# Kernel optimization log

Hardware: AMD Instinct MI355X
Metric: run time of the kernel (lower is better)

Reference implementation:

```python
import jax, jax.numpy as jnp
import numpy as np

D = 768       # feature dim (LayerNorm([768]))
NCHAR = 96    # codebook rows (char_dic = zeros(96, 768))
EPS = 1e-5    # torch LayerNorm default eps
EMA = 0.1     # EMA update coefficient


def layer_norm(x, w, b):
    mu = jnp.mean(x, axis=-1, keepdims=True)
    var = jnp.mean((x - mu) ** 2, axis=-1, keepdims=True)
    return (x - mu) * jax.lax.rsqrt(var + EPS) * w + b


def setup_inputs() -> dict:
    key = jax.random.key(0)
    k1, k2, k3 = jax.random.split(key, 3)
    B, S = 128, 1024
    return {
        "input_f": jax.random.normal(k1, (B, S, D), dtype=jnp.float32),
        "char_dic": jax.random.normal(k2, (NCHAR, D), dtype=jnp.float32),
        "ln_w": jnp.ones((D,), dtype=jnp.float32),
        "ln_b": jnp.zeros((D,), dtype=jnp.float32),
        "target": jax.random.randint(k3, (B, S), 0, NCHAR),
    }


def reference(input_f, char_dic, ln_w, ln_b, target):
    x = layer_norm(input_f, ln_w, ln_b)              # [B, S, D]
    flat = x.reshape(-1, D)                          # [N, D]
    labels = target.reshape(-1)                      # [N]
    # per-label scatter-add of token embeddings
    tok_sums = jax.ops.segment_sum(flat, labels, num_segments=NCHAR)          # [96, D]
    counts = jax.ops.segment_sum(jnp.ones_like(labels, dtype=jnp.float32),
                                 labels, num_segments=NCHAR)                  # [96]
    # group i = [char_dic[i]] + tokens with label i; row-sum of that group:
    group_sum = char_dic + tok_sums
    # sum of all pairwise dot products within a group == ||row-sum||^2
    positive = jnp.sum(group_sum * group_sum) / D
    # EMA codebook update (rows 1..95 only; row 0 untouched)
    mean = group_sum / (counts + 1.0)[:, None]       # group size = n_i + 1 (dic row)
    upd = char_dic + EMA * mean
    new_char = jnp.where(jnp.arange(NCHAR)[:, None] >= 1, upd, char_dic)
    # torch applies layer_norm1 to the updated codebook under no_grad
    normed = jax.lax.stop_gradient(layer_norm(new_char, ln_w, ln_b))
    s = jnp.sum(normed[1:], axis=0)                  # sum-of-rows identity again
    negative = jnp.dot(s, s) / D
    return negative - positive
```

## Files before the change

### kernel.cpp

```cpp
#include <hip/hip_runtime.h>

#define DD 768
#define NCH 96
#define NTOK 16
#define NBLK 128

__device__ __forceinline__ float wave_reduce_sum(float v) {
#pragma unroll
  for (int m = 32; m >= 1; m >>= 1) v += __shfl_xor(v, m, 64);
  return v;
}

__global__ void __launch_bounds__(256) k_prep(const int* __restrict__ tgt, int n, int chunk,
                                              float* __restrict__ zbase, int* __restrict__ phist) {
  __shared__ int lh[NCH];
  int tid = threadIdx.x, bid = blockIdx.x;
  if (tid < NCH) lh[tid] = 0;
  int gi = bid * 256 + tid;
  if (gi < 800) zbase[gi] = 0.f;
  __syncthreads();
  int beg = bid * chunk, end = min(beg + chunk, n);
  for (int i = beg + tid; i < end; i += 256) atomicAdd(&lh[tgt[i]], 1);
  __syncthreads();
  if (tid < NCH) phist[bid * NCH + tid] = lh[tid];
}

__global__ void __launch_bounds__(256) k_scatter(const int* __restrict__ tgt, int n, int chunk,
                                                 const int* __restrict__ phist,
                                                 int* __restrict__ sorted,
                                                 int* __restrict__ offs_g, int* __restrict__ sbase_g,
                                                 int* __restrict__ nslots,
                                                 int* __restrict__ tbase, int* __restrict__ tcnt) {
  __shared__ int tot[NCH], cbase[NCH], lcnt[NCH];
  __shared__ int offs_l[NCH + 1], sb_l[NCH + 1];
  int tid = threadIdx.x, bid = blockIdx.x;
  if (tid < NCH) {
    int s = 0, p = 0;
    for (int b = 0; b < NBLK; ++b) {
      int v = phist[b * NCH + tid];
      s += v;
      if (b < bid) p += v;
    }
    tot[tid] = s; cbase[tid] = p; lcnt[tid] = 0;
  }
  __syncthreads();
  if (tid == 0) {
    int off = 0, sb = 0;
    for (int c = 0; c < NCH; ++c) {
      offs_l[c] = off; sb_l[c] = sb;
      off += tot[c]; sb += (tot[c] + NTOK - 1) / NTOK;
    }
    offs_l[NCH] = off; sb_l[NCH] = sb;
  }
  __syncthreads();
  if (bid == 0) {
    for (int c = tid; c <= NCH; c += 256) { offs_g[c] = offs_l[c]; sbase_g[c] = sb_l[c]; }
    if (tid == 0) *nslots = sb_l[NCH];
    for (int c = tid; c < NCH; c += 256) {
      int o = offs_l[c], ncnt = tot[c], sb = sb_l[c];
      int nsl = (ncnt + NTOK - 1) / NTOK;
      for (int j = 0; j < nsl; ++j) {
        tbase[sb + j] = o + j * NTOK;
        tcnt[sb + j] = min(NTOK, ncnt - j * NTOK);
      }
    }
  }
  int beg = bid * chunk, end = min(beg + chunk, n);
  for (int i = beg + tid; i < end; i += 256) {
    int c = tgt[i];
    int r = atomicAdd(&lcnt[c], 1);
    sorted[offs_l[c] + cbase[c] + r] = i;
  }
}

__global__ void __launch_bounds__(256) k_main(
    const float* __restrict__ x, const int* __restrict__ sorted,
    const int* __restrict__ tbase, const int* __restrict__ tcnt,
    const int* __restrict__ nslots,
    float* __restrict__ P, float* __restrict__ Pm) {
  int lane = threadIdx.x & 63;
  int w = (blockIdx.x * blockDim.x + threadIdx.x) >> 6;
  int W = (gridDim.x * blockDim.x) >> 6;
  int S = *nslots;
  for (int s = w; s < S; s += W) {
    int base = tbase[s], cnt = tcnt[s];
    int tl = (lane < cnt) ? sorted[base + lane] : 0;
    int t = __shfl(tl, 0);
    const float4* r0 = (const float4*)(x + (size_t)t * DD);
    float4 A = r0[lane], B = r0[64 + lane], C = r0[128 + lane];
    float acc[12];
#pragma unroll
    for (int k = 0; k < 12; ++k) acc[k] = 0.f;
    float mcp = 0.f;
    for (int i = 0; i < cnt; ++i) {
      float4 An, Bn, Cn;
      if (i + 1 < cnt) {
        int tn = __shfl(tl, i + 1);
        const float4* rn = (const float4*)(x + (size_t)tn * DD);
        An = rn[lane]; Bn = rn[64 + lane]; Cn = rn[128 + lane];
      }
      float v[12] = {A.x, A.y, A.z, A.w, B.x, B.y, B.z, B.w, C.x, C.y, C.z, C.w};
      float ssum = 0.f, q = 0.f;
#pragma unroll
      for (int k = 0; k < 12; ++k) { ssum += v[k]; q += v[k] * v[k]; }
      ssum = wave_reduce_sum(ssum);
      q = wave_reduce_sum(q);
      float mu = ssum * (1.f / DD);
      float var = q * (1.f / DD) - mu * mu;
      float rstd = rsqrtf(var + 1e-5f);
#pragma unroll
      for (int k = 0; k < 12; ++k) acc[k] += rstd * v[k];
      mcp += rstd * mu;
      A = An; B = Bn; C = Cn;
    }
    float4* Pr = (float4*)(P + (size_t)s * DD);
    Pr[lane]       = make_float4(acc[0], acc[1], acc[2], acc[3]);
    Pr[64 + lane]  = make_float4(acc[4], acc[5], acc[6], acc[7]);
    Pr[128 + lane] = make_float4(acc[8], acc[9], acc[10], acc[11]);
    if (lane == 0) Pm[s] = mcp;
  }
}

__global__ void __launch_bounds__(256) k_finish(
    const float* __restrict__ dic, const float* __restrict__ wv_,
    const float* __restrict__ bv_, const float* __restrict__ P,
    const float* __restrict__ Pm, const int* __restrict__ offs_g,
    const int* __restrict__ sbase_g,
    float* __restrict__ gS, float* __restrict__ gpos, int* __restrict__ counter,
    float* __restrict__ out) {
  __shared__ float accsh[DD];
  __shared__ float mcsh;
  int c = blockIdx.x, tid = threadIdx.x, lane = tid & 63, wid = tid >> 6;
  for (int i = tid; i < DD; i += 256) accsh[i] = 0.f;
  if (tid == 0) mcsh = 0.f;
  __syncthreads();
  int sb = sbase_g[c], se = sbase_g[c + 1];
  float nc = (float)(offs_g[c + 1] - offs_g[c]);
  float acc[12];
#pragma unroll
  for (int k = 0; k < 12; ++k) acc[k] = 0.f;
  float mcp = 0.f;
  for (int s = sb + wid; s < se; s += 4) {
    const float4* Pr = (const float4*)(P + (size_t)s * DD);
    float4 A = Pr[lane], B = Pr[64 + lane], C = Pr[128 + lane];
    acc[0] += A.x; acc[1] += A.y; acc[2]  += A.z; acc[3]  += A.w;
    acc[4] += B.x; acc[5] += B.y; acc[6]  += B.z; acc[7]  += B.w;
    acc[8] += C.x; acc[9] += C.y; acc[10] += C.z; acc[11] += C.w;
    mcp += Pm[s];
  }
#pragma unroll
  for (int k = 0; k < 12; ++k) {
    int d = (k >> 2) * 256 + 4 * lane + (k & 3);
    atomicAdd(&accsh[d], acc[k]);
  }
  if (lane == 0) atomicAdd(&mcsh, mcp);
  __syncthreads();
  if (wid == 0) {
    float mc = mcsh;
    float g[12], pacc = 0.f;
#pragma unroll
    for (int k = 0; k < 12; ++k) {
      int d = (k >> 2) * 256 + 4 * lane + (k & 3);
      float gg = dic[c * DD + d] + wv_[d] * (accsh[d] - mc) + nc * bv_[d];
      g[k] = gg; pacc += gg * gg;
    }
    pacc = wave_reduce_sum(pacc);
    if (lane == 0) atomicAdd(gpos, pacc);
    if (c >= 1) {
      float inv = 1.f / (nc + 1.f);
      float u[12], sum = 0.f, sq = 0.f;
#pragma unroll
      for (int k = 0; k < 12; ++k) {
        int d = (k >> 2) * 256 + 4 * lane + (k & 3);
        float uu = dic[c * DD + d] + 0.1f * g[k] * inv;
        u[k] = uu; sum += uu; sq += uu * uu;
      }
      sum = wave_reduce_sum(sum);
      sq = wave_reduce_sum(sq);
      float mu = sum * (1.f / DD);
      float rstd = rsqrtf(sq * (1.f / DD) - mu * mu + 1e-5f);
#pragma unroll
      for (int k = 0; k < 12; ++k) {
        int d = (k >> 2) * 256 + 4 * lane + (k & 3);
        atomicAdd(&gS[d], (u[k] - mu) * rstd * wv_[d] + bv_[d]);
      }
    }
    __threadfence();
    int done = 0;
    if (lane == 0) done = (atomicAdd(counter, 1) == NCH - 1) ? 1 : 0;
    done = __shfl(done, 0);
    if (done) {
      __threadfence();
      float nv = 0.f;
#pragma unroll
      for (int k = 0; k < 12; ++k) {
        int d = (k >> 2) * 256 + 4 * lane + (k & 3);
        float t = gS[d];
        nv += t * t;
      }
      nv = wave_reduce_sum(nv);
      if (lane == 0) out[0] = (nv - gpos[0]) * (1.f / DD);
    }
  }
}

extern "C" void kernel_launch(void* const* d_in, const int* in_sizes, int n_in,
                              void* d_out, int out_size, void* d_ws, size_t ws_size,
                              hipStream_t stream) {
  (void)n_in; (void)out_size; (void)ws_size;
  const float* x   = (const float*)d_in[0];
  const float* dic = (const float*)d_in[1];
  const float* w   = (const float*)d_in[2];
  const float* b   = (const float*)d_in[3];
  const int*   tgt = (const int*)d_in[4];
  float* out = (float*)d_out;
  int N = in_sizes[4];

  char* ws = (char*)d_ws;
  float* gS      = (float*)(ws);
  float* gpos    = (float*)(ws + 3072);
  int*   counter = (int*)(ws + 3076);
  int*   offs_g  = (int*)(ws + 3200);
  int*   sbase_g = (int*)(ws + 3648);
  int*   nslots  = (int*)(ws + 4096);
  int*   tbase   = (int*)(ws + 4160);

  int maxslots = (N + NTOK - 1) / NTOK + NCH;
  size_t o_tcnt = 4160 + (size_t)maxslots * 4;
  int*   tcnt = (int*)(ws + o_tcnt);
  size_t o_pm = o_tcnt + (size_t)maxslots * 4;
  float* Pm = (float*)(ws + o_pm);
  size_t o_ph = o_pm + (size_t)maxslots * 4;
  int*   phist = (int*)(ws + o_ph);
  size_t o_P = (o_ph + (size_t)NBLK * NCH * 4 + 255) & ~(size_t)255;
  float* P = (float*)(ws + o_P);
  size_t o_sorted = o_P + (size_t)maxslots * DD * 4;
  int*   sorted = (int*)(ws + o_sorted);

  int chunk = (N + NBLK - 1) / NBLK;
  k_prep<<<NBLK, 256, 0, stream>>>(tgt, N, chunk, (float*)ws, phist);
  k_scatter<<<NBLK, 256, 0, stream>>>(tgt, N, chunk, phist, sorted,
                                      offs_g, sbase_g, nslots, tbase, tcnt);
  k_main<<<1024, 256, 0, stream>>>(x, sorted, tbase, tcnt, nslots, P, Pm);
  k_finish<<<NCH, 256, 0, stream>>>(dic, w, b, P, Pm, offs_g, sbase_g,
                                    gS, gpos, counter, out);
}
```

Before: 139.5 us.

## Fuse main and finish kernels with last-block ticket handoff, unroll full slots

```diff
diff --git a/kernel.cpp b/kernel.cpp
--- a/kernel.cpp
+++ b/kernel.cpp
@@ -4,6 +4,7 @@
 #define NCH 96
 #define NTOK 16
 #define NBLK 128
+#define MGRID 1024
 
 __device__ __forceinline__ float wave_reduce_sum(float v) {
 #pragma unroll
@@ -17,7 +18,7 @@
   int tid = threadIdx.x, bid = blockIdx.x;
   if (tid < NCH) lh[tid] = 0;
   int gi = bid * 256 + tid;
-  if (gi < 800) zbase[gi] = 0.f;
+  if (gi < 1024) zbase[gi] = 0.f;
   __syncthreads();
   int beg = bid * chunk, end = min(beg + chunk, n);
   for (int i = beg + tid; i < end; i += 256) atomicAdd(&lh[tgt[i]], 1);
@@ -73,45 +74,52 @@
   }
 }
 
-__global__ void __launch_bounds__(256) k_main(
+__device__ __forceinline__ void proc_row(const float* __restrict__ x, int t, int lane,
+                                         float acc[12], float& mcp) {
+  const float4* r = (const float4*)(x + (size_t)t * DD);
+  float4 A = r[lane], B = r[64 + lane], C = r[128 + lane];
+  float v[12] = {A.x, A.y, A.z, A.w, B.x, B.y, B.z, B.w, C.x, C.y, C.z, C.w};
+  float s = 0.f, q = 0.f;
+#pragma unroll
+  for (int k = 0; k < 12; ++k) { s += v[k]; q += v[k] * v[k]; }
+  s = wave_reduce_sum(s);
+  q = wave_reduce_sum(q);
+  float mu = s * (1.f / DD);
+  float rstd = rsqrtf(q * (1.f / DD) - mu * mu + 1e-5f);
+#pragma unroll
+  for (int k = 0; k < 12; ++k) acc[k] += rstd * v[k];
+  mcp += rstd * mu;
+}
+
+__global__ void __launch_bounds__(256, 4) k_mainfin(
     const float* __restrict__ x, const int* __restrict__ sorted,
     const int* __restrict__ tbase, const int* __restrict__ tcnt,
     const int* __restrict__ nslots,
-    float* __restrict__ P, float* __restrict__ Pm) {
-  int lane = threadIdx.x & 63;
-  int w = (blockIdx.x * blockDim.x + threadIdx.x) >> 6;
+    float* __restrict__ P, float* __restrict__ Pm,
+    const float* __restrict__ dic, const float* __restrict__ wv_,
+    const float* __restrict__ bv_,
+    const int* __restrict__ offs_g, const int* __restrict__ sbase_g,
+    float* __restrict__ gS, float* __restrict__ gpos,
+    int* __restrict__ ctr1, int* __restrict__ ctr2,
+    float* __restrict__ out) {
+  __shared__ int sh_t;
+  int tid = threadIdx.x, lane = tid & 63;
+  int w = (blockIdx.x * blockDim.x + tid) >> 6;
   int W = (gridDim.x * blockDim.x) >> 6;
   int S = *nslots;
+
   for (int s = w; s < S; s += W) {
     int base = tbase[s], cnt = tcnt[s];
     int tl = (lane < cnt) ? sorted[base + lane] : 0;
-    int t = __shfl(tl, 0);
-    const float4* r0 = (const float4*)(x + (size_t)t * DD);
-    float4 A = r0[lane], B = r0[64 + lane], C = r0[128 + lane];
     float acc[12];
 #pragma unroll
     for (int k = 0; k < 12; ++k) acc[k] = 0.f;
     float mcp = 0.f;
-    for (int i = 0; i < cnt; ++i) {
-      float4 An, Bn, Cn;
-      if (i + 1 < cnt) {
-        int tn = __shfl(tl, i + 1);
-        const float4* rn = (const float4*)(x + (size_t)tn * DD);
-        An = rn[lane]; Bn = rn[64 + lane]; Cn = rn[128 + lane];
-      }
-      float v[12] = {A.x, A.y, A.z, A.w, B.x, B.y, B.z, B.w, C.x, C.y, C.z, C.w};
-      float ssum = 0.f, q = 0.f;
-#pragma unroll
-      for (int k = 0; k < 12; ++k) { ssum += v[k]; q += v[k] * v[k]; }
-      ssum = wave_reduce_sum(ssum);
-      q = wave_reduce_sum(q);
-      float mu = ssum * (1.f / DD);
-      float var = q * (1.f / DD) - mu * mu;
-      float rstd = rsqrtf(var + 1e-5f);
-#pragma unroll
-      for (int k = 0; k < 12; ++k) acc[k] += rstd * v[k];
-      mcp += rstd * mu;
-      A = An; B = Bn; C = Cn;
+    if (cnt == NTOK) {
+#pragma unroll
+      for (int i = 0; i < NTOK; ++i) proc_row(x, __shfl(tl, i), lane, acc, mcp);
+    } else {
+      for (int i = 0; i < cnt; ++i) proc_row(x, __shfl(tl, i), lane, acc, mcp);
     }
     float4* Pr = (float4*)(P + (size_t)s * DD);
     Pr[lane]       = make_float4(acc[0], acc[1], acc[2], acc[3]);
@@ -119,18 +127,23 @@
     Pr[128 + lane] = make_float4(acc[8], acc[9], acc[10], acc[11]);
     if (lane == 0) Pm[s] = mcp;
   }
-}
-
-__global__ void __launch_bounds__(256) k_finish(
-    const float* __restrict__ dic, const float* __restrict__ wv_,
-    const float* __restrict__ bv_, const float* __restrict__ P,
-    const float* __restrict__ Pm, const int* __restrict__ offs_g,
-    const int* __restrict__ sbase_g,
-    float* __restrict__ gS, float* __restrict__ gpos, int* __restrict__ counter,
-    float* __restrict__ out) {
+
+  __syncthreads();
+  if (tid == 0) { __threadfence(); sh_t = atomicAdd(ctr1, 1); }
+  __syncthreads();
+  int tk = sh_t;
+  int G = gridDim.x;
+  if (tk < G - NCH) return;
+  int c = tk - (G - NCH);
+  if (tid == 0) {
+    while (atomicAdd(ctr1, 0) < G) __builtin_amdgcn_s_sleep(8);
+  }
+  __syncthreads();
+  __threadfence();
+
   __shared__ float accsh[DD];
   __shared__ float mcsh;
-  int c = blockIdx.x, tid = threadIdx.x, lane = tid & 63, wid = tid >> 6;
+  int wid = tid >> 6;
   for (int i = tid; i < DD; i += 256) accsh[i] = 0.f;
   if (tid == 0) mcsh = 0.f;
   __syncthreads();
@@ -187,7 +200,7 @@
     }
     __threadfence();
     int done = 0;
-    if (lane == 0) done = (atomicAdd(counter, 1) == NCH - 1) ? 1 : 0;
+    if (lane == 0) done = (atomicAdd(ctr2, 1) == NCH - 1) ? 1 : 0;
     done = __shfl(done, 0);
     if (done) {
       __threadfence();
@@ -219,14 +232,16 @@
   char* ws = (char*)d_ws;
   float* gS      = (float*)(ws);
   float* gpos    = (float*)(ws + 3072);
-  int*   counter = (int*)(ws + 3076);
-  int*   offs_g  = (int*)(ws + 3200);
-  int*   sbase_g = (int*)(ws + 3648);
-  int*   nslots  = (int*)(ws + 4096);
-  int*   tbase   = (int*)(ws + 4160);
+  int*   ctr1    = (int*)(ws + 3076);
+  int*   ctr2    = (int*)(ws + 3080);
+  int*   offs_g  = (int*)(ws + 4096);
+  int*   sbase_g = (int*)(ws + 4544);
+  int*   nslots  = (int*)(ws + 4992);
 
   int maxslots = (N + NTOK - 1) / NTOK + NCH;
-  size_t o_tcnt = 4160 + (size_t)maxslots * 4;
+  size_t o_tbase = 5120;
+  int*   tbase = (int*)(ws + o_tbase);
+  size_t o_tcnt = o_tbase + (size_t)maxslots * 4;
   int*   tcnt = (int*)(ws + o_tcnt);
   size_t o_pm = o_tcnt + (size_t)maxslots * 4;
   float* Pm = (float*)(ws + o_pm);
@@ -241,7 +256,7 @@
   k_prep<<<NBLK, 256, 0, stream>>>(tgt, N, chunk, (float*)ws, phist);
   k_scatter<<<NBLK, 256, 0, stream>>>(tgt, N, chunk, phist, sorted,
                                       offs_g, sbase_g, nslots, tbase, tcnt);
-  k_main<<<1024, 256, 0, stream>>>(x, sorted, tbase, tcnt, nslots, P, Pm);
-  k_finish<<<NCH, 256, 0, stream>>>(dic, w, b, P, Pm, offs_g, sbase_g,
-                                    gS, gpos, counter, out);
-}
+  k_mainfin<<<MGRID, 256, 0, stream>>>(x, sorted, tbase, tcnt, nslots, P, Pm,
+                                       dic, w, b, offs_g, sbase_g,
+                                       gS, gpos, ctr1, ctr2, out);
+}
```

Result: slower. 260.6 us (+86.9%).
